# Kernel tuning notes

Measured on AMD Instinct MI355X. Metric: run time of the kernel, lower is better.

The kernel has to match this reference:

```python
import jax, jax.numpy as jnp
import numpy as np

B, S, I, H, O = 512, 256, 32, 256, 24
EPS = 1e-5


def setup_inputs() -> dict:
    key = jax.random.key(0)
    ks = jax.random.split(key, 8)
    sc = 0.05
    return {
        "x": jax.random.normal(ks[0], (B, S, I), dtype=jnp.float32),
        "W_in": jax.random.normal(ks[1], (H, I), dtype=jnp.float32) * sc,
        "b_in": jnp.zeros((H,), dtype=jnp.float32),
        "W": jax.random.normal(ks[2], (4 * H, 2 * H), dtype=jnp.float32) * sc,
        "R": jax.random.normal(ks[3], (4 * H, H), dtype=jnp.float32) * sc,
        "b": jnp.zeros((4 * H,), dtype=jnp.float32),
        "W_out": jax.random.normal(ks[4], (O, H), dtype=jnp.float32) * sc,
        "b_out": jnp.zeros((O,), dtype=jnp.float32),
    }


def _slstm_forward(x, W_in, b_in, W, R, b, W_out, b_out):
    h_dim = W_in.shape[0]
    bsz = x.shape[0]
    # input projection: [B,S,H]
    xp = jnp.einsum("bsi,hi->bsh", x, W_in) + b_in
    # W acts on cat(x_t, h): split into x-part and h-part; fold recurrent R in
    Wx = W[:, :h_dim]          # [4H, H]
    Whr = W[:, h_dim:] + R     # [4H, H]
    xt = jnp.swapaxes(xp, 0, 1)  # [S,B,H]

    z0 = jnp.zeros((bsz, h_dim), dtype=x.dtype)
    init = (z0, z0, z0, z0)  # h, c, n, m

    def step(carry, x_t):
        h, c, n, m = carry
        gates = x_t @ Wx.T + h @ Whr.T + b  # [B,4H]
        i_raw, f_raw, z_raw, o_raw = jnp.split(gates, 4, axis=-1)
        f = jax.nn.sigmoid(f_raw)
        log_f = jnp.log(f)
        # stabilizer: m = max(log f + m, log i) with log i == i_raw
        m_new = jnp.maximum(log_f + m, i_raw)
        i_p = jnp.exp(i_raw - m_new)
        f_p = jnp.exp(log_f + m - m_new)
        c_new = f_p * c + i_p * jnp.tanh(z_raw)
        n_new = f_p * n + i_p
        h_new = jax.nn.sigmoid(o_raw) * jnp.tanh(c_new / n_new)
        return (h_new, c_new, n_new, m_new), None

    (h, _, _, _), _ = jax.lax.scan(step, init, xt)
    out = h @ W_out.T + b_out  # [B,O]
    # InstanceNorm1d (no affine): per-sample normalization over output dim
    mu = out.mean(axis=-1, keepdims=True)
    var = ((out - mu) ** 2).mean(axis=-1, keepdims=True)
    return (out - mu) / jnp.sqrt(var + EPS)


def reference(x, W_in, b_in, W, R, b, W_out, b_out):
    return _slstm_forward(x, W_in, b_in, W, R, b, W_out, b_out)
```

## Files before the change

kernel.cpp:

```cpp
#include <hip/hip_runtime.h>
#include <hip/hip_bf16.h>

constexpr int Bs = 512;
constexpr int Ss = 256;
constexpr int Is = 32;
constexpr int Hs = 256;
constexpr int Os = 24;
constexpr int MB = 16;
constexpr int NBLK = Bs / MB;
constexpr int NTH = 512;

typedef __attribute__((ext_vector_type(8))) short short8;
typedef __attribute__((ext_vector_type(4))) float f32x4;

#define DEV static __device__ __forceinline__

DEV short f2bf(float f) {
  __hip_bfloat16 h = __float2bfloat16(f);
  short s;
  __builtin_memcpy(&s, &h, 2);
  return s;
}

DEV float frcp(float x) { return __builtin_amdgcn_rcpf(x); }

DEV float tanh_fast(float x) {
  x = fminf(fmaxf(x, -15.f), 15.f);
  float u = __expf(2.f * x);
  return (u - 1.f) * frcp(u + 1.f);
}

DEV short8 ldg8(const short* p) { return *reinterpret_cast<const short8*>(p); }

DEV float xvf(uint2 v, int r) {
  unsigned wd = (r & 2) ? v.y : v.x;
  unsigned bits = ((r & 1) ? (wd >> 16) : (wd & 0xffffu)) << 16;
  float f;
  __builtin_memcpy(&f, &bits, 4);
  return f;
}

__global__ void prep_wstream(const float* __restrict__ W, const float* __restrict__ R,
                             short* __restrict__ wst) {
  int tid = blockIdx.x * 256 + threadIdx.x;
  int j  = tid & 7;
  int l  = (tid >> 3) & 63;
  int kt = (tid >> 9) & 7;
  int nt = (tid >> 12) & 7;
  int w  = tid >> 15;
  int n = l & 15, kg = (l >> 4) & 3;
  int g = nt & 3, half = (nt >> 2) & 1;
  int gr = g * 256 + w * 32 + half * 16 + n;
  int k  = kt * 32 + kg * 8 + j;
  float v = W[gr * 512 + 256 + k] + R[gr * 256 + k];
  wst[tid] = f2bf(v);
}

__global__ void prep_weff(const float* __restrict__ W, const float* __restrict__ W_in,
                          short* __restrict__ weff) {
  int tid = blockIdx.x * 256 + threadIdx.x;
  int j  = tid & 7;
  int l  = (tid >> 3) & 63;
  int nt = (tid >> 9) & 7;
  int w  = tid >> 12;
  int n = l & 15, kg = (l >> 4) & 3;
  int g = nt & 3, half = (nt >> 2) & 1;
  int gr = g * 256 + w * 32 + half * 16 + n;
  int i  = kg * 8 + j;
  float acc = 0.f;
  for (int h = 0; h < Hs; ++h) acc += W[gr * 512 + h] * W_in[h * 32 + i];
  weff[tid] = f2bf(acc);
}

__global__ void prep_bfrag(const float* __restrict__ W, const float* __restrict__ b,
                           const float* __restrict__ b_in, float* __restrict__ bf) {
  int tid = blockIdx.x * 256 + threadIdx.x;
  int l = tid & 63, nt = (tid >> 6) & 7, w = tid >> 9;
  int g = nt & 3, half = (nt >> 2) & 1;
  int gr = g * 256 + w * 32 + half * 16 + (l & 15);
  float a = b[gr];
  for (int h = 0; h < Hs; ++h) a += W[gr * 512 + h] * b_in[h];
  bf[tid] = a;
}

DEV void chunk_gemm(const float* __restrict__ x, const short* __restrict__ weffF,
                    const float* __restrict__ bfrag, short* __restrict__ xps,
                    int b0, int w, int l, int t0, int tc) {
  const int l15 = l & 15, lhi = l >> 4;
  float bv[8];
#pragma unroll
  for (int nt = 0; nt < 8; ++nt) bv[nt] = bfrag[(w * 8 + nt) * 64 + l];
  short8 wf[8];
#pragma unroll
  for (int nt = 0; nt < 8; ++nt) wf[nt] = ldg8(weffF + ((w * 8 + nt) * 64 + l) * 8);
  const float* px0 = x + (size_t)(b0 + l15) * (Ss * Is) + lhi * 8;
  for (int tt = 0; tt < tc; ++tt) {
    const float* px = px0 + (size_t)(t0 + tt) * Is;
    f32x4 a0 = *(const f32x4*)px;
    f32x4 a1 = *(const f32x4*)(px + 4);
    short8 xa;
#pragma unroll
    for (int j = 0; j < 4; ++j) { xa[j] = f2bf(a0[j]); xa[4 + j] = f2bf(a1[j]); }
    short* xo = xps + (size_t)tt * 16384 + (size_t)(w * 8) * 256 + l * 4;
#pragma unroll
    for (int nt = 0; nt < 8; ++nt) {
      f32x4 c = {bv[nt], bv[nt], bv[nt], bv[nt]};
      c = __builtin_amdgcn_mfma_f32_16x16x32_bf16(xa, wf[nt], c, 0, 0, 0);
      unsigned lo = ((unsigned)(unsigned short)f2bf(c[1]) << 16) | (unsigned short)f2bf(c[0]);
      unsigned hi = ((unsigned)(unsigned short)f2bf(c[3]) << 16) | (unsigned short)f2bf(c[2]);
      uint2 v; v.x = lo; v.y = hi;
      *reinterpret_cast<uint2*>(xo + (size_t)nt * 256) = v;
    }
  }
}

template <bool INLINE_X>
__global__ __launch_bounds__(NTH, 2) void slstm_main(
    const float* __restrict__ x,
    const short* __restrict__ Wst,
    const short* __restrict__ WeffF,
    const float* __restrict__ Bfrag,
    const float* __restrict__ Wout,
    const float* __restrict__ bout,
    short* __restrict__ xp,
    float* __restrict__ out,
    int tc)
{
  extern __shared__ char smem[];
  short* hbuf = reinterpret_cast<short*>(smem);
  short* wlds = reinterpret_cast<short*>(smem + 16384);

  const int tid = threadIdx.x;
  const int w   = tid >> 6;
  const int l   = tid & 63;
  const int lg  = l >> 4;
  const int n16 = l & 15;
  const int bb  = blockIdx.x;
  const int b0  = bb * MB;

  const short* wsb = Wst + (size_t)(w * 64) * 512 + l * 8;
  const f32x4 zero4 = {0.f, 0.f, 0.f, 0.f};

  short8 wreg[48];
#pragma unroll
  for (int kt = 0; kt < 6; ++kt)
#pragma unroll
    for (int nt = 0; nt < 8; ++nt)
      wreg[kt * 8 + nt] = ldg8(wsb + (nt * 8 + kt) * 512);

#pragma unroll
  for (int f = 0; f < 16; ++f) {
    int kt = 6 + (f >> 3), nt = f & 7;
    short8 v = ldg8(wsb + (nt * 8 + kt) * 512);
    *reinterpret_cast<short8*>(&wlds[(w * 16 + f) * 512 + l * 8]) = v;
  }

  float bv[8];
  if constexpr (INLINE_X) {
#pragma unroll
    for (int nt = 0; nt < 8; ++nt) bv[nt] = Bfrag[(w * 8 + nt) * 64 + l];
  }

  {
    short8 z = {0, 0, 0, 0, 0, 0, 0, 0};
    *reinterpret_cast<short8*>(&hbuf[tid * 8]) = z;
  }

  float cst[8], nst[8], mst[8];
#pragma unroll
  for (int s = 0; s < 8; ++s) { cst[s] = 0.f; nst[s] = 0.f; mst[s] = 0.f; }

  short* xp_blk = xp + (size_t)bb * tc * 16384;

  __syncthreads();

  for (int t0 = 0; t0 < Ss; t0 += tc) {
    if constexpr (!INLINE_X) {
      if (tc < Ss) {
        chunk_gemm(x, WeffF, Bfrag, xp_blk, b0, w, l, t0, tc);
        __syncthreads();
      }
    }
    for (int tt = 0; tt < tc; ++tt) {
      const int t = t0 + tt, pb = t & 1;

      short8 xa, wfx[8];
      if constexpr (INLINE_X) {
        const float* px = x + (size_t)(b0 + n16) * (Ss * Is) + (size_t)t * Is + lg * 8;
        f32x4 a0 = *(const f32x4*)px;
        f32x4 a1 = *(const f32x4*)(px + 4);
#pragma unroll
        for (int j = 0; j < 4; ++j) { xa[j] = f2bf(a0[j]); xa[4 + j] = f2bf(a1[j]); }
#pragma unroll
        for (int nt = 0; nt < 8; ++nt) wfx[nt] = ldg8(WeffF + ((w * 8 + nt) * 64 + l) * 8);
      }

#pragma unroll
      for (int half = 0; half < 2; ++half) {
        f32x4 acc[4];
        uint2 xv[4];
        if constexpr (!INLINE_X) {
          const short* xq = xp_blk + (size_t)tt * 16384 + (w * 8 + half * 4) * 256 + l * 4;
#pragma unroll
          for (int g = 0; g < 4; ++g) xv[g] = *reinterpret_cast<const uint2*>(xq + g * 256);
#pragma unroll
          for (int g = 0; g < 4; ++g) acc[g] = zero4;
        } else {
#pragma unroll
          for (int g = 0; g < 4; ++g) {
            float b = bv[half * 4 + g];
            f32x4 c = {b, b, b, b};
            acc[g] = __builtin_amdgcn_mfma_f32_16x16x32_bf16(xa, wfx[half * 4 + g], c, 0, 0, 0);
          }
        }
#pragma unroll
        for (int kt = 0; kt < 6; ++kt) {
          short8 ha = *reinterpret_cast<const short8*>(
              &hbuf[pb * 4096 + n16 * 256 + (((kt * 4 + lg) ^ n16) & 31) * 8]);
#pragma unroll
          for (int g = 0; g < 4; ++g)
            acc[g] = __builtin_amdgcn_mfma_f32_16x16x32_bf16(ha, wreg[kt * 8 + half * 4 + g], acc[g], 0, 0, 0);
        }
#pragma unroll
        for (int kt = 6; kt < 8; ++kt) {
          short8 ha = *reinterpret_cast<const short8*>(
              &hbuf[pb * 4096 + n16 * 256 + (((kt * 4 + lg) ^ n16) & 31) * 8]);
#pragma unroll
          for (int g = 0; g < 4; ++g) {
            short8 wf = *reinterpret_cast<const short8*>(
                &wlds[(w * 16 + (kt - 6) * 8 + half * 4 + g) * 512 + l * 8]);
            acc[g] = __builtin_amdgcn_mfma_f32_16x16x32_bf16(ha, wf, acc[g], 0, 0, 0);
          }
        }
#pragma unroll
        for (int r = 0; r < 4; ++r) {
          const int s = half * 4 + r;
          float xi = acc[0][r];
          float xf = acc[1][r];
          float xz = acc[2][r];
          float xo = acc[3][r];
          if constexpr (!INLINE_X) {
            xi += xvf(xv[0], r); xf += xvf(xv[1], r);
            xz += xvf(xv[2], r); xo += xvf(xv[3], r);
          }
          float lf = -__logf(1.f + __expf(-xf));
          float mn = fmaxf(lf + mst[s], xi);
          float ip = __expf(xi - mn);
          float fp = __expf(lf + mst[s] - mn);
          float tz = tanh_fast(xz);
          float cn  = fp * cst[s] + ip * tz;
          float nn2 = fp * nst[s] + ip;
          cst[s] = cn; nst[s] = nn2; mst[s] = mn;
          float so = frcp(1.f + __expf(-xo));
          float hv = so * tanh_fast(cn * frcp(nn2));
          int j  = w * 32 + half * 16 + n16;
          int bi = lg * 4 + r;
          hbuf[(pb ^ 1) * 4096 + bi * 256 + (((j >> 3) ^ bi) & 31) * 8 + (j & 7)] = f2bf(hv);
        }
      }
      __syncthreads();
    }
  }

  float* h32 = reinterpret_cast<float*>(smem + 16384);
#pragma unroll
  for (int half = 0; half < 2; ++half)
#pragma unroll
    for (int r = 0; r < 4; ++r) {
      int j = w * 32 + half * 16 + n16, bi = lg * 4 + r;
      unsigned short u = (unsigned short)hbuf[bi * 256 + (((j >> 3) ^ bi) & 31) * 8 + (j & 7)];
      unsigned bits = (unsigned)u << 16;
      float hv;
      __builtin_memcpy(&hv, &bits, 4);
      h32[bi * 256 + j] = hv;
    }
  __syncthreads();

  float* olds = reinterpret_cast<float*>(smem + 32768);
  if (tid < MB * Os) {
    int bi = tid / Os, o = tid % Os;
    const float* wrow = Wout + o * Hs;
    const float* hrow = h32 + bi * Hs;
    float acc = bout[o];
#pragma unroll 4
    for (int jj = 0; jj < Hs; jj += 4) {
      f32x4 hv = *(const f32x4*)(hrow + jj);
      f32x4 wv = *(const f32x4*)(wrow + jj);
      acc += hv[0] * wv[0] + hv[1] * wv[1] + hv[2] * wv[2] + hv[3] * wv[3];
    }
    olds[bi * Os + o] = acc;
  }
  __syncthreads();

  if (tid < MB) {
    float mu = 0.f;
#pragma unroll
    for (int o = 0; o < Os; ++o) mu += olds[tid * Os + o];
    mu *= (1.f / Os);
    float var = 0.f;
#pragma unroll
    for (int o = 0; o < Os; ++o) { float d = olds[tid * Os + o] - mu; var += d * d; }
    var *= (1.f / Os);
    float inv = rsqrtf(var + 1e-5f);
    for (int o = 0; o < Os; ++o)
      out[(size_t)(b0 + tid) * Os + o] = (olds[tid * Os + o] - mu) * inv;
  }
}

extern "C" void kernel_launch(void* const* d_in, const int* in_sizes, int n_in,
                              void* d_out, int out_size, void* d_ws, size_t ws_size,
                              hipStream_t stream) {
  const float* x    = (const float*)d_in[0];
  const float* W_in = (const float*)d_in[1];
  const float* b_in = (const float*)d_in[2];
  const float* W    = (const float*)d_in[3];
  const float* R    = (const float*)d_in[4];
  const float* bb_  = (const float*)d_in[5];
  const float* Wout = (const float*)d_in[6];
  const float* bout = (const float*)d_in[7];
  float* out = (float*)d_out;

  short* wst   = (short*)d_ws;
  short* weff  = (short*)((char*)d_ws + 524288);
  float* bfrag = (float*)((char*)d_ws + 589824);
  short* xp    = (short*)((char*)d_ws + 655360);

  int tc = 16;
  while (tc > 0 && (size_t)tc * 1048576 + 655360 > ws_size) tc >>= 1;

  prep_wstream<<<1024, 256, 0, stream>>>(W, R, wst);
  prep_weff<<<128, 256, 0, stream>>>(W, W_in, weff);
  prep_bfrag<<<16, 256, 0, stream>>>(W, bb_, b_in, bfrag);

  if (tc > 0) {
    hipFuncSetAttribute(reinterpret_cast<const void*>(slstm_main<false>),
                        hipFuncAttributeMaxDynamicSharedMemorySize, 147456);
    slstm_main<false><<<NBLK, NTH, 147456, stream>>>(x, wst, weff, bfrag, Wout, bout,
                                                     xp, out, tc);
  } else {
    hipFuncSetAttribute(reinterpret_cast<const void*>(slstm_main<true>),
                        hipFuncAttributeMaxDynamicSharedMemorySize, 147456);
    slstm_main<true><<<NBLK, NTH, 147456, stream>>>(x, wst, weff, bfrag, Wout, bout,
                                                    xp, out, Ss);
  }
}
```

Measured before the change: 1.439 ms.

## Precompute full input projection in separate kernel and stream last weight tile from global

After: 1.603 ms. +11.4%, slower.

```diff
diff --git a/kernel.cpp b/kernel.cpp
--- a/kernel.cpp
+++ b/kernel.cpp
@@ -56,6 +56,12 @@
   wst[tid] = f2bf(v);
 }
 
+__global__ void prep_dup7(const short* __restrict__ wst, short* __restrict__ dup) {
+  int tid = blockIdx.x * 256 + threadIdx.x;
+  int q = tid >> 9, r = tid & 511;
+  dup[tid] = wst[(q * 8 + 7) * 512 + r];
+}
+
 __global__ void prep_weff(const float* __restrict__ W, const float* __restrict__ W_in,
                           short* __restrict__ weff) {
   int tid = blockIdx.x * 256 + threadIdx.x;
@@ -114,10 +120,21 @@
   }
 }
 
-template <bool INLINE_X>
+__global__ __launch_bounds__(NTH) void xp_pre(const float* __restrict__ x,
+                                              const short* __restrict__ weffF,
+                                              const float* __restrict__ bfrag,
+                                              short* __restrict__ xp) {
+  int bb = blockIdx.x & 31, ch = blockIdx.x >> 5;
+  int w = threadIdx.x >> 6, l = threadIdx.x & 63;
+  short* xps = xp + (size_t)bb * 256 * 16384 + (size_t)ch * 16 * 16384;
+  chunk_gemm(x, weffF, bfrag, xps, bb * MB, w, l, ch * 16, 16);
+}
+
+template <bool CHUNKED>
 __global__ __launch_bounds__(NTH, 2) void slstm_main(
     const float* __restrict__ x,
     const short* __restrict__ Wst,
+    const short* __restrict__ Wdup,
     const short* __restrict__ WeffF,
     const float* __restrict__ Bfrag,
     const float* __restrict__ Wout,
@@ -138,27 +155,22 @@
   const int bb  = blockIdx.x;
   const int b0  = bb * MB;
 
-  const short* wsb = Wst + (size_t)(w * 64) * 512 + l * 8;
+  const short* wsb   = Wst  + (size_t)(w * 64) * 512 + l * 8;
+  const short* wdupb = Wdup + (size_t)(w * 8) * 512 + l * 8;
   const f32x4 zero4 = {0.f, 0.f, 0.f, 0.f};
 
-  short8 wreg[48];
-#pragma unroll
-  for (int kt = 0; kt < 6; ++kt)
+  short8 wreg[40];
+#pragma unroll
+  for (int kt = 0; kt < 5; ++kt)
 #pragma unroll
     for (int nt = 0; nt < 8; ++nt)
       wreg[kt * 8 + nt] = ldg8(wsb + (nt * 8 + kt) * 512);
 
 #pragma unroll
   for (int f = 0; f < 16; ++f) {
-    int kt = 6 + (f >> 3), nt = f & 7;
+    int kt = 5 + (f >> 3), nt = f & 7;
     short8 v = ldg8(wsb + (nt * 8 + kt) * 512);
     *reinterpret_cast<short8*>(&wlds[(w * 16 + f) * 512 + l * 8]) = v;
-  }
-
-  float bv[8];
-  if constexpr (INLINE_X) {
-#pragma unroll
-    for (int nt = 0; nt < 8; ++nt) bv[nt] = Bfrag[(w * 8 + nt) * 64 + l];
   }
 
   {
@@ -175,46 +187,34 @@
   __syncthreads();
 
   for (int t0 = 0; t0 < Ss; t0 += tc) {
-    if constexpr (!INLINE_X) {
-      if (tc < Ss) {
-        chunk_gemm(x, WeffF, Bfrag, xp_blk, b0, w, l, t0, tc);
-        __syncthreads();
-      }
+    if constexpr (CHUNKED) {
+      chunk_gemm(x, WeffF, Bfrag, xp_blk, b0, w, l, t0, tc);
+      __syncthreads();
     }
     for (int tt = 0; tt < tc; ++tt) {
       const int t = t0 + tt, pb = t & 1;
-
-      short8 xa, wfx[8];
-      if constexpr (INLINE_X) {
-        const float* px = x + (size_t)(b0 + n16) * (Ss * Is) + (size_t)t * Is + lg * 8;
-        f32x4 a0 = *(const f32x4*)px;
-        f32x4 a1 = *(const f32x4*)(px + 4);
-#pragma unroll
-        for (int j = 0; j < 4; ++j) { xa[j] = f2bf(a0[j]); xa[4 + j] = f2bf(a1[j]); }
-#pragma unroll
-        for (int nt = 0; nt < 8; ++nt) wfx[nt] = ldg8(WeffF + ((w * 8 + nt) * 64 + l) * 8);
-      }
+      asm volatile("" ::: "memory");
 
 #pragma unroll
       for (int half = 0; half < 2; ++half) {
+        short8 w7[4];
+#pragma unroll
+        for (int g = 0; g < 4; ++g) {
+          const short* p7 = (t & 1) ? (wdupb + (half * 4 + g) * 512)
+                                    : (wsb + ((half * 4 + g) * 8 + 7) * 512);
+          w7[g] = ldg8(p7);
+        }
+        const short* xq = xp_blk + (size_t)tt * 16384 + (w * 8 + half * 4) * 256 + l * 4;
+        uint2 xv[4];
+#pragma unroll
+        for (int g = 0; g < 4; ++g) xv[g] = *reinterpret_cast<const uint2*>(xq + g * 256);
+
         f32x4 acc[4];
-        uint2 xv[4];
-        if constexpr (!INLINE_X) {
-          const short* xq = xp_blk + (size_t)tt * 16384 + (w * 8 + half * 4) * 256 + l * 4;
-#pragma unroll
-          for (int g = 0; g < 4; ++g) xv[g] = *reinterpret_cast<const uint2*>(xq + g * 256);
-#pragma unroll
-          for (int g = 0; g < 4; ++g) acc[g] = zero4;
-        } else {
-#pragma unroll
-          for (int g = 0; g < 4; ++g) {
-            float b = bv[half * 4 + g];
-            f32x4 c = {b, b, b, b};
-            acc[g] = __builtin_amdgcn_mfma_f32_16x16x32_bf16(xa, wfx[half * 4 + g], c, 0, 0, 0);
-          }
-        }
-#pragma unroll
-        for (int kt = 0; kt < 6; ++kt) {
+#pragma unroll
+        for (int g = 0; g < 4; ++g) acc[g] = zero4;
+
+#pragma unroll
+        for (int kt = 0; kt < 5; ++kt) {
           short8 ha = *reinterpret_cast<const short8*>(
               &hbuf[pb * 4096 + n16 * 256 + (((kt * 4 + lg) ^ n16) & 31) * 8]);
 #pragma unroll
@@ -222,27 +222,31 @@
             acc[g] = __builtin_amdgcn_mfma_f32_16x16x32_bf16(ha, wreg[kt * 8 + half * 4 + g], acc[g], 0, 0, 0);
         }
 #pragma unroll
-        for (int kt = 6; kt < 8; ++kt) {
+        for (int kt = 5; kt < 7; ++kt) {
           short8 ha = *reinterpret_cast<const short8*>(
               &hbuf[pb * 4096 + n16 * 256 + (((kt * 4 + lg) ^ n16) & 31) * 8]);
 #pragma unroll
           for (int g = 0; g < 4; ++g) {
             short8 wf = *reinterpret_cast<const short8*>(
-                &wlds[(w * 16 + (kt - 6) * 8 + half * 4 + g) * 512 + l * 8]);
+                &wlds[(w * 16 + (kt - 5) * 8 + half * 4 + g) * 512 + l * 8]);
             acc[g] = __builtin_amdgcn_mfma_f32_16x16x32_bf16(ha, wf, acc[g], 0, 0, 0);
           }
         }
+        {
+          short8 ha = *reinterpret_cast<const short8*>(
+              &hbuf[pb * 4096 + n16 * 256 + (((7 * 4 + lg) ^ n16) & 31) * 8]);
+#pragma unroll
+          for (int g = 0; g < 4; ++g)
+            acc[g] = __builtin_amdgcn_mfma_f32_16x16x32_bf16(ha, w7[g], acc[g], 0, 0, 0);
+        }
+
 #pragma unroll
         for (int r = 0; r < 4; ++r) {
           const int s = half * 4 + r;
-          float xi = acc[0][r];
-          float xf = acc[1][r];
-          float xz = acc[2][r];
-          float xo = acc[3][r];
-          if constexpr (!INLINE_X) {
-            xi += xvf(xv[0], r); xf += xvf(xv[1], r);
-            xz += xvf(xv[2], r); xo += xvf(xv[3], r);
-          }
+          float xi = acc[0][r] + xvf(xv[0], r);
+          float xf = acc[1][r] + xvf(xv[1], r);
+          float xz = acc[2][r] + xvf(xv[2], r);
+          float xo = acc[3][r] + xvf(xv[3], r);
           float lf = -__logf(1.f + __expf(-xf));
           float mn = fmaxf(lf + mst[s], xi);
           float ip = __expf(xi - mn);
@@ -321,26 +325,36 @@
   float* out = (float*)d_out;
 
   short* wst   = (short*)d_ws;
-  short* weff  = (short*)((char*)d_ws + 524288);
-  float* bfrag = (float*)((char*)d_ws + 589824);
-  short* xp    = (short*)((char*)d_ws + 655360);
-
-  int tc = 16;
-  while (tc > 0 && (size_t)tc * 1048576 + 655360 > ws_size) tc >>= 1;
+  short* wdup  = (short*)((char*)d_ws + 524288);
+  short* weff  = (short*)((char*)d_ws + 655360);
+  float* bfrag = (float*)((char*)d_ws + 720896);
+  short* xp    = (short*)((char*)d_ws + 1048576);
+
+  const size_t XP_FULL = 268435456ull;
+  bool full = ws_size >= 1048576ull + XP_FULL;
+  int tc;
+  if (full) {
+    tc = Ss;
+  } else {
+    tc = 16;
+    while (tc > 1 && (size_t)tc * 1048576ull + 1048576ull > ws_size) tc >>= 1;
+  }
 
   prep_wstream<<<1024, 256, 0, stream>>>(W, R, wst);
+  prep_dup7<<<256, 256, 0, stream>>>(wst, wdup);
   prep_weff<<<128, 256, 0, stream>>>(W, W_in, weff);
   prep_bfrag<<<16, 256, 0, stream>>>(W, bb_, b_in, bfrag);
 
-  if (tc > 0) {
+  if (full) {
+    xp_pre<<<512, NTH, 0, stream>>>(x, weff, bfrag, xp);
     hipFuncSetAttribute(reinterpret_cast<const void*>(slstm_main<false>),
                         hipFuncAttributeMaxDynamicSharedMemorySize, 147456);
-    slstm_main<false><<<NBLK, NTH, 147456, stream>>>(x, wst, weff, bfrag, Wout, bout,
-                                                     xp, out, tc);
+    slstm_main<false><<<NBLK, NTH, 147456, stream>>>(x, wst, wdup, weff, bfrag,
+                                                     Wout, bout, xp, out, tc);
   } else {
     hipFuncSetAttribute(reinterpret_cast<const void*>(slstm_main<true>),
                         hipFuncAttributeMaxDynamicSharedMemorySize, 147456);
-    slstm_main<true><<<NBLK, NTH, 147456, stream>>>(x, wst, weff, bfrag, Wout, bout,
-                                                    xp, out, Ss);
-  }
-}
+    slstm_main<true><<<NBLK, NTH, 147456, stream>>>(x, wst, wdup, weff, bfrag,
+                                                    Wout, bout, xp, out, tc);
+  }
+}
```

## Halve waves per block, widen per-wave gate tiles, and simplify the stabilizer math

Applied to the files above, without the earlier changes.

Result: slower. 2.833 ms (+96.9%).

```diff
diff --git a/kernel.cpp b/kernel.cpp
--- a/kernel.cpp
+++ b/kernel.cpp
@@ -8,7 +8,7 @@
 constexpr int Os = 24;
 constexpr int MB = 16;
 constexpr int NBLK = Bs / MB;
-constexpr int NTH = 512;
+constexpr int NTH = 256;
 
 typedef __attribute__((ext_vector_type(8))) short short8;
 typedef __attribute__((ext_vector_type(4))) float f32x4;
@@ -46,11 +46,10 @@
   int j  = tid & 7;
   int l  = (tid >> 3) & 63;
   int kt = (tid >> 9) & 7;
-  int nt = (tid >> 12) & 7;
-  int w  = tid >> 15;
+  int q  = tid >> 12;
   int n = l & 15, kg = (l >> 4) & 3;
-  int g = nt & 3, half = (nt >> 2) & 1;
-  int gr = g * 256 + w * 32 + half * 16 + n;
+  int g = q & 3, hg = q >> 2;
+  int gr = g * 256 + hg * 16 + n;
   int k  = kt * 32 + kg * 8 + j;
   float v = W[gr * 512 + 256 + k] + R[gr * 256 + k];
   wst[tid] = f2bf(v);
@@ -61,11 +60,10 @@
   int tid = blockIdx.x * 256 + threadIdx.x;
   int j  = tid & 7;
   int l  = (tid >> 3) & 63;
-  int nt = (tid >> 9) & 7;
-  int w  = tid >> 12;
+  int q  = tid >> 9;
   int n = l & 15, kg = (l >> 4) & 3;
-  int g = nt & 3, half = (nt >> 2) & 1;
-  int gr = g * 256 + w * 32 + half * 16 + n;
+  int g = q & 3, hg = q >> 2;
+  int gr = g * 256 + hg * 16 + n;
   int i  = kg * 8 + j;
   float acc = 0.f;
   for (int h = 0; h < Hs; ++h) acc += W[gr * 512 + h] * W_in[h * 32 + i];
@@ -75,47 +73,48 @@
 __global__ void prep_bfrag(const float* __restrict__ W, const float* __restrict__ b,
                            const float* __restrict__ b_in, float* __restrict__ bf) {
   int tid = blockIdx.x * 256 + threadIdx.x;
-  int l = tid & 63, nt = (tid >> 6) & 7, w = tid >> 9;
-  int g = nt & 3, half = (nt >> 2) & 1;
-  int gr = g * 256 + w * 32 + half * 16 + (l & 15);
+  int l = tid & 63, q = tid >> 6;
+  int g = q & 3, hg = q >> 2;
+  int gr = g * 256 + hg * 16 + (l & 15);
   float a = b[gr];
   for (int h = 0; h < Hs; ++h) a += W[gr * 512 + h] * b_in[h];
   bf[tid] = a;
 }
 
-DEV void chunk_gemm(const float* __restrict__ x, const short* __restrict__ weffF,
-                    const float* __restrict__ bfrag, short* __restrict__ xps,
-                    int b0, int w, int l, int t0, int tc) {
+template <int TC>
+DEV void chunk_gemm4(const float* __restrict__ x, const short* __restrict__ weffF,
+                     const float* __restrict__ bfrag, short* __restrict__ xps,
+                     int b0, int w, int l, int t0) {
   const int l15 = l & 15, lhi = l >> 4;
-  float bv[8];
-#pragma unroll
-  for (int nt = 0; nt < 8; ++nt) bv[nt] = bfrag[(w * 8 + nt) * 64 + l];
-  short8 wf[8];
-#pragma unroll
-  for (int nt = 0; nt < 8; ++nt) wf[nt] = ldg8(weffF + ((w * 8 + nt) * 64 + l) * 8);
+  short8 xa[TC];
   const float* px0 = x + (size_t)(b0 + l15) * (Ss * Is) + lhi * 8;
-  for (int tt = 0; tt < tc; ++tt) {
+#pragma unroll
+  for (int tt = 0; tt < TC; ++tt) {
     const float* px = px0 + (size_t)(t0 + tt) * Is;
     f32x4 a0 = *(const f32x4*)px;
     f32x4 a1 = *(const f32x4*)(px + 4);
-    short8 xa;
-#pragma unroll
-    for (int j = 0; j < 4; ++j) { xa[j] = f2bf(a0[j]); xa[4 + j] = f2bf(a1[j]); }
-    short* xo = xps + (size_t)tt * 16384 + (size_t)(w * 8) * 256 + l * 4;
-#pragma unroll
-    for (int nt = 0; nt < 8; ++nt) {
-      f32x4 c = {bv[nt], bv[nt], bv[nt], bv[nt]};
-      c = __builtin_amdgcn_mfma_f32_16x16x32_bf16(xa, wf[nt], c, 0, 0, 0);
+#pragma unroll
+    for (int j = 0; j < 4; ++j) { xa[tt][j] = f2bf(a0[j]); xa[tt][4 + j] = f2bf(a1[j]); }
+  }
+#pragma unroll
+  for (int nt = 0; nt < 16; ++nt) {
+    int q = w * 16 + nt;
+    short8 wf = ldg8(weffF + (size_t)q * 512 + l * 8);
+    float bv = bfrag[q * 64 + l];
+#pragma unroll
+    for (int tt = 0; tt < TC; ++tt) {
+      f32x4 c = {bv, bv, bv, bv};
+      c = __builtin_amdgcn_mfma_f32_16x16x32_bf16(xa[tt], wf, c, 0, 0, 0);
       unsigned lo = ((unsigned)(unsigned short)f2bf(c[1]) << 16) | (unsigned short)f2bf(c[0]);
       unsigned hi = ((unsigned)(unsigned short)f2bf(c[3]) << 16) | (unsigned short)f2bf(c[2]);
       uint2 v; v.x = lo; v.y = hi;
-      *reinterpret_cast<uint2*>(xo + (size_t)nt * 256) = v;
+      *reinterpret_cast<uint2*>(xps + (size_t)tt * 16384 + (size_t)q * 256 + l * 4) = v;
     }
   }
 }
 
-template <bool INLINE_X>
-__global__ __launch_bounds__(NTH, 2) void slstm_main(
+template <int TC>
+__global__ __launch_bounds__(NTH, 1) void slstm_main(
     const float* __restrict__ x,
     const short* __restrict__ Wst,
     const short* __restrict__ WeffF,
@@ -123,8 +122,7 @@
     const float* __restrict__ Wout,
     const float* __restrict__ bout,
     short* __restrict__ xp,
-    float* __restrict__ out,
-    int tc)
+    float* __restrict__ out)
 {
   extern __shared__ char smem[];
   short* hbuf = reinterpret_cast<short*>(smem);
@@ -138,122 +136,94 @@
   const int bb  = blockIdx.x;
   const int b0  = bb * MB;
 
-  const short* wsb = Wst + (size_t)(w * 64) * 512 + l * 8;
+  const short* wsb = Wst + (size_t)(w * 16 * 8) * 512 + l * 8;
   const f32x4 zero4 = {0.f, 0.f, 0.f, 0.f};
 
-  short8 wreg[48];
-#pragma unroll
-  for (int kt = 0; kt < 6; ++kt)
-#pragma unroll
-    for (int nt = 0; nt < 8; ++nt)
-      wreg[kt * 8 + nt] = ldg8(wsb + (nt * 8 + kt) * 512);
-
-#pragma unroll
-  for (int f = 0; f < 16; ++f) {
-    int kt = 6 + (f >> 3), nt = f & 7;
-    short8 v = ldg8(wsb + (nt * 8 + kt) * 512);
-    *reinterpret_cast<short8*>(&wlds[(w * 16 + f) * 512 + l * 8]) = v;
-  }
-
-  float bv[8];
-  if constexpr (INLINE_X) {
-#pragma unroll
-    for (int nt = 0; nt < 8; ++nt) bv[nt] = Bfrag[(w * 8 + nt) * 64 + l];
+  short8 wreg[96];
+#pragma unroll
+  for (int ql = 0; ql < 16; ++ql)
+#pragma unroll
+    for (int kt = 0; kt < 6; ++kt)
+      wreg[ql * 6 + kt] = ldg8(wsb + (ql * 8 + kt) * 512);
+
+#pragma unroll
+  for (int f = 0; f < 32; ++f) {
+    int kt = 6 + (f >> 4), ql = f & 15;
+    short8 v = ldg8(wsb + (ql * 8 + kt) * 512);
+    *reinterpret_cast<short8*>(&wlds[(w * 32 + f) * 512 + l * 8]) = v;
   }
 
   {
     short8 z = {0, 0, 0, 0, 0, 0, 0, 0};
-    *reinterpret_cast<short8*>(&hbuf[tid * 8]) = z;
-  }
-
-  float cst[8], nst[8], mst[8];
-#pragma unroll
-  for (int s = 0; s < 8; ++s) { cst[s] = 0.f; nst[s] = 0.f; mst[s] = 0.f; }
-
-  short* xp_blk = xp + (size_t)bb * tc * 16384;
+    for (int i = tid; i < 512; i += NTH)
+      *reinterpret_cast<short8*>(&hbuf[i * 8]) = z;
+  }
+
+  float cst[16], nst[16], mst[16];
+#pragma unroll
+  for (int s = 0; s < 16; ++s) { cst[s] = 0.f; nst[s] = 0.f; mst[s] = 0.f; }
+
+  short* xp_blk = xp + (size_t)bb * TC * 16384;
 
   __syncthreads();
 
-  for (int t0 = 0; t0 < Ss; t0 += tc) {
-    if constexpr (!INLINE_X) {
-      if (tc < Ss) {
-        chunk_gemm(x, WeffF, Bfrag, xp_blk, b0, w, l, t0, tc);
-        __syncthreads();
-      }
-    }
-    for (int tt = 0; tt < tc; ++tt) {
+#pragma unroll 1
+  for (int t0 = 0; t0 < Ss; t0 += TC) {
+    chunk_gemm4<TC>(x, WeffF, Bfrag, xp_blk, b0, w, l, t0);
+
+#pragma unroll 1
+    for (int tt = 0; tt < TC; ++tt) {
       const int t = t0 + tt, pb = t & 1;
 
-      short8 xa, wfx[8];
-      if constexpr (INLINE_X) {
-        const float* px = x + (size_t)(b0 + n16) * (Ss * Is) + (size_t)t * Is + lg * 8;
-        f32x4 a0 = *(const f32x4*)px;
-        f32x4 a1 = *(const f32x4*)(px + 4);
-#pragma unroll
-        for (int j = 0; j < 4; ++j) { xa[j] = f2bf(a0[j]); xa[4 + j] = f2bf(a1[j]); }
-#pragma unroll
-        for (int nt = 0; nt < 8; ++nt) wfx[nt] = ldg8(WeffF + ((w * 8 + nt) * 64 + l) * 8);
-      }
-
-#pragma unroll
-      for (int half = 0; half < 2; ++half) {
+#pragma unroll
+      for (int hh = 0; hh < 4; ++hh) {
+        const short* xq = xp_blk + (size_t)tt * 16384 + (size_t)(w * 16 + hh * 4) * 256 + l * 4;
+        uint2 xv[4];
+#pragma unroll
+        for (int g = 0; g < 4; ++g) xv[g] = *reinterpret_cast<const uint2*>(xq + g * 256);
+
         f32x4 acc[4];
-        uint2 xv[4];
-        if constexpr (!INLINE_X) {
-          const short* xq = xp_blk + (size_t)tt * 16384 + (w * 8 + half * 4) * 256 + l * 4;
-#pragma unroll
-          for (int g = 0; g < 4; ++g) xv[g] = *reinterpret_cast<const uint2*>(xq + g * 256);
-#pragma unroll
-          for (int g = 0; g < 4; ++g) acc[g] = zero4;
-        } else {
-#pragma unroll
-          for (int g = 0; g < 4; ++g) {
-            float b = bv[half * 4 + g];
-            f32x4 c = {b, b, b, b};
-            acc[g] = __builtin_amdgcn_mfma_f32_16x16x32_bf16(xa, wfx[half * 4 + g], c, 0, 0, 0);
+#pragma unroll
+        for (int g = 0; g < 4; ++g) acc[g] = zero4;
+
+#pragma unroll
+        for (int kt = 0; kt < 8; ++kt) {
+          short8 ha = *reinterpret_cast<const short8*>(
+              &hbuf[pb * 4096 + n16 * 256 + (((kt * 4 + lg) ^ n16) & 31) * 8]);
+          if (kt < 6) {
+#pragma unroll
+            for (int g = 0; g < 4; ++g)
+              acc[g] = __builtin_amdgcn_mfma_f32_16x16x32_bf16(
+                  ha, wreg[(hh * 4 + g) * 6 + kt], acc[g], 0, 0, 0);
+          } else {
+#pragma unroll
+            for (int g = 0; g < 4; ++g) {
+              short8 wf = *reinterpret_cast<const short8*>(
+                  &wlds[(w * 32 + (kt - 6) * 16 + hh * 4 + g) * 512 + l * 8]);
+              acc[g] = __builtin_amdgcn_mfma_f32_16x16x32_bf16(ha, wf, acc[g], 0, 0, 0);
+            }
           }
         }
-#pragma unroll
-        for (int kt = 0; kt < 6; ++kt) {
-          short8 ha = *reinterpret_cast<const short8*>(
-              &hbuf[pb * 4096 + n16 * 256 + (((kt * 4 + lg) ^ n16) & 31) * 8]);
-#pragma unroll
-          for (int g = 0; g < 4; ++g)
-            acc[g] = __builtin_amdgcn_mfma_f32_16x16x32_bf16(ha, wreg[kt * 8 + half * 4 + g], acc[g], 0, 0, 0);
-        }
-#pragma unroll
-        for (int kt = 6; kt < 8; ++kt) {
-          short8 ha = *reinterpret_cast<const short8*>(
-              &hbuf[pb * 4096 + n16 * 256 + (((kt * 4 + lg) ^ n16) & 31) * 8]);
-#pragma unroll
-          for (int g = 0; g < 4; ++g) {
-            short8 wf = *reinterpret_cast<const short8*>(
-                &wlds[(w * 16 + (kt - 6) * 8 + half * 4 + g) * 512 + l * 8]);
-            acc[g] = __builtin_amdgcn_mfma_f32_16x16x32_bf16(ha, wf, acc[g], 0, 0, 0);
-          }
-        }
+
 #pragma unroll
         for (int r = 0; r < 4; ++r) {
-          const int s = half * 4 + r;
-          float xi = acc[0][r];
-          float xf = acc[1][r];
-          float xz = acc[2][r];
-          float xo = acc[3][r];
-          if constexpr (!INLINE_X) {
-            xi += xvf(xv[0], r); xf += xvf(xv[1], r);
-            xz += xvf(xv[2], r); xo += xvf(xv[3], r);
-          }
-          float lf = -__logf(1.f + __expf(-xf));
-          float mn = fmaxf(lf + mst[s], xi);
+          const int s = hh * 4 + r;
+          float xi = acc[0][r] + xvf(xv[0], r);
+          float xf = acc[1][r] + xvf(xv[1], r);
+          float xz = acc[2][r] + xvf(xv[2], r);
+          float xo = acc[3][r] + xvf(xv[3], r);
+          float mo = mst[s];
+          float mn = fmaxf(mo, xi);
           float ip = __expf(xi - mn);
-          float fp = __expf(lf + mst[s] - mn);
+          float fs = frcp(1.f + __expf(-xf));
+          float fp = fs * __expf(mo - mn);
           float tz = tanh_fast(xz);
           float cn  = fp * cst[s] + ip * tz;
           float nn2 = fp * nst[s] + ip;
           cst[s] = cn; nst[s] = nn2; mst[s] = mn;
           float so = frcp(1.f + __expf(-xo));
           float hv = so * tanh_fast(cn * frcp(nn2));
-          int j  = w * 32 + half * 16 + n16;
+          int j  = w * 64 + hh * 16 + n16;
           int bi = lg * 4 + r;
           hbuf[(pb ^ 1) * 4096 + bi * 256 + (((j >> 3) ^ bi) & 31) * 8 + (j & 7)] = f2bf(hv);
         }
@@ -264,10 +234,10 @@
 
   float* h32 = reinterpret_cast<float*>(smem + 16384);
 #pragma unroll
-  for (int half = 0; half < 2; ++half)
+  for (int hh = 0; hh < 4; ++hh)
 #pragma unroll
     for (int r = 0; r < 4; ++r) {
-      int j = w * 32 + half * 16 + n16, bi = lg * 4 + r;
+      int j = w * 64 + hh * 16 + n16, bi = lg * 4 + r;
       unsigned short u = (unsigned short)hbuf[bi * 256 + (((j >> 3) ^ bi) & 31) * 8 + (j & 7)];
       unsigned bits = (unsigned)u << 16;
       float hv;
@@ -277,8 +247,8 @@
   __syncthreads();
 
   float* olds = reinterpret_cast<float*>(smem + 32768);
-  if (tid < MB * Os) {
-    int bi = tid / Os, o = tid % Os;
+  for (int oi = tid; oi < MB * Os; oi += NTH) {
+    int bi = oi / Os, o = oi % Os;
     const float* wrow = Wout + o * Hs;
     const float* hrow = h32 + bi * Hs;
     float acc = bout[o];
@@ -325,22 +295,18 @@
   float* bfrag = (float*)((char*)d_ws + 589824);
   short* xp    = (short*)((char*)d_ws + 655360);
 
-  int tc = 16;
-  while (tc > 0 && (size_t)tc * 1048576 + 655360 > ws_size) tc >>= 1;
-
   prep_wstream<<<1024, 256, 0, stream>>>(W, R, wst);
   prep_weff<<<128, 256, 0, stream>>>(W, W_in, weff);
   prep_bfrag<<<16, 256, 0, stream>>>(W, bb_, b_in, bfrag);
 
-  if (tc > 0) {
-    hipFuncSetAttribute(reinterpret_cast<const void*>(slstm_main<false>),
+  bool tc8 = ws_size >= 655360ull + 8ull * 1048576ull;
+  if (tc8) {
+    hipFuncSetAttribute(reinterpret_cast<const void*>(slstm_main<8>),
                         hipFuncAttributeMaxDynamicSharedMemorySize, 147456);
-    slstm_main<false><<<NBLK, NTH, 147456, stream>>>(x, wst, weff, bfrag, Wout, bout,
-                                                     xp, out, tc);
+    slstm_main<8><<<NBLK, NTH, 147456, stream>>>(x, wst, weff, bfrag, Wout, bout, xp, out);
   } else {
-    hipFuncSetAttribute(reinterpret_cast<const void*>(slstm_main<true>),
+    hipFuncSetAttribute(reinterpret_cast<const void*>(slstm_main<1>),
                         hipFuncAttributeMaxDynamicSharedMemorySize, 147456);
-    slstm_main<true><<<NBLK, NTH, 147456, stream>>>(x, wst, weff, bfrag, Wout, bout,
-                                                    xp, out, Ss);
-  }
-}
+    slstm_main<1><<<NBLK, NTH, 147456, stream>>>(x, wst, weff, bfrag, Wout, bout, xp, out);
+  }
+}
```
